# Kernel optimization log

Hardware: AMD Instinct MI355X
Metric: run time of the kernel (lower is better)

## Reference

```python
import jax, jax.numpy as jnp
import numpy as np

Q_OFFSET = 128  # stored quants are in [0,255); subtract to get signed int8 range


def setup_inputs() -> dict:
    key = jax.random.key(0)
    k1, k2, k3, k4 = jax.random.split(key, 4)
    O, NB, BS = 4096, 128, 32  # out_features, num_blocks, block_size (Q8_0)
    x = jax.random.normal(k1, (4, 1024, NB * BS), dtype=jnp.float16)
    q_weight = jax.random.randint(k2, (O, NB, BS), 0, 255, dtype=jnp.int32)
    scales = jax.random.uniform(k3, (O, NB), dtype=jnp.float16) * jnp.float16(0.05)
    bias = jax.random.normal(k4, (O,), dtype=jnp.float16)
    return {"x": x, "q_weight": q_weight, "scales": scales, "bias": bias}


def reference(x, q_weight, scales, bias):
    # GGUF Q8_0-style on-the-fly dequant: w[o, b*32+j] = (q[o,b,j]-128) * scale[o,b]
    q = q_weight.astype(jnp.float16) - jnp.float16(Q_OFFSET)  # [O, NB, BS]
    w = (q * scales[:, :, None]).reshape(scales.shape[0], -1)  # [O, I]
    # linear: y = x @ w^T + bias
    return jnp.einsum('bsi,oi->bso', x, w) + bias
```

## Files before the change

kernel.cpp:

```cpp
#include <hip/hip_runtime.h>
#include <stdint.h>


#define QOFF 128

typedef __bf16 bf16_t;
typedef __bf16 bf16x8 __attribute__((ext_vector_type(8)));
typedef float f32x4 __attribute__((ext_vector_type(4)));

__global__ __launch_bounds__(256) void prep_kernel(
    const int* __restrict__ q, const float* __restrict__ scales,
    const float* __restrict__ X, bf16_t* __restrict__ W,
    bf16_t* __restrict__ Xb, int K, int NB, int nDeq) {
  const int b = blockIdx.x;
  if (b < nDeq) {
    const size_t e = ((size_t)b * 256 + threadIdx.x) * 8;
    const int o = (int)(e / (size_t)K);
    const int i = (int)(e % (size_t)K);
    const float s = scales[o * NB + (i >> 5)];
    int4 a = *(const int4*)(q + e);
    int4 c = *(const int4*)(q + e + 4);
    const int* av = (const int*)&a;
    const int* cv = (const int*)&c;
    bf16x8 t;
#pragma unroll
    for (int j = 0; j < 4; ++j) t[j] = (bf16_t)((float)(av[j] - QOFF) * s);
#pragma unroll
    for (int j = 0; j < 4; ++j) t[4 + j] = (bf16_t)((float)(cv[j] - QOFF) * s);
    *(bf16x8*)(W + e) = t;
  } else {
    const size_t e = ((size_t)(b - nDeq) * 256 + threadIdx.x) * 8;
    float4 a = *(const float4*)(X + e);
    float4 c = *(const float4*)(X + e + 4);
    bf16x8 t;
    t[0] = (bf16_t)a.x; t[1] = (bf16_t)a.y; t[2] = (bf16_t)a.z; t[3] = (bf16_t)a.w;
    t[4] = (bf16_t)c.x; t[5] = (bf16_t)c.y; t[6] = (bf16_t)c.z; t[7] = (bf16_t)c.w;
    *(bf16x8*)(Xb + e) = t;
  }
}

__device__ __forceinline__ void async16(bf16_t* lds, const bf16_t* g) {
  __builtin_amdgcn_global_load_lds(
      (const __attribute__((address_space(1))) unsigned int*)(const void*)g,
      (__attribute__((address_space(3))) unsigned int*)(void*)lds, 16, 0, 0);
}

__global__ __launch_bounds__(256) void gemm_db(
    const bf16_t* __restrict__ A,
    const bf16_t* __restrict__ B,
    const float* __restrict__ bias,
    float* __restrict__ C,
    int M, int N, int K) {
  __shared__ bf16_t lsA[2][128 * 32];
  __shared__ bf16_t lsB[2][128 * 32];

  const int tid = threadIdx.x;
  const int lane = tid & 63;
  const int wave = tid >> 6;
  const int m0 = blockIdx.y * 128;
  const int n0 = blockIdx.x * 128;
  const int wm = (wave >> 1) * 64;
  const int wn = (wave & 1) * 64;
  const int r = lane & 15;
  const int qd = lane >> 4;

  f32x4 acc[4][4] = {};

  const int e0 = tid * 8;
  const int e1 = 2048 + tid * 8;
  const int r0 = e0 >> 5, c0 = e0 & 31;
  const int r1 = e1 >> 5, c1 = e1 & 31;

  const bf16_t* gA0 = A + (size_t)(m0 + r0) * K + c0;
  const bf16_t* gA1 = A + (size_t)(m0 + r1) * K + c1;
  const bf16_t* gB0 = B + (size_t)(n0 + r0) * K + c0;
  const bf16_t* gB1 = B + (size_t)(n0 + r1) * K + c1;

  async16(&lsA[0][e0], gA0);
  async16(&lsA[0][e1], gA1);
  async16(&lsB[0][e0], gB0);
  async16(&lsB[0][e1], gB1);

  int buf = 0;
  for (int k0 = 0; k0 < K; k0 += 32, buf ^= 1) {
    __syncthreads();
    if (k0 + 32 < K) {
      const int nk = k0 + 32;
      async16(&lsA[buf ^ 1][e0], gA0 + nk);
      async16(&lsA[buf ^ 1][e1], gA1 + nk);
      async16(&lsB[buf ^ 1][e0], gB0 + nk);
      async16(&lsB[buf ^ 1][e1], gB1 + nk);
    }

    bf16x8 af[4], bfv[4];
#pragma unroll
    for (int i = 0; i < 4; ++i) {
      af[i] = *(const bf16x8*)&lsA[buf][(wm + i * 16 + r) * 32 + qd * 8];
      bfv[i] = *(const bf16x8*)&lsB[buf][(wn + i * 16 + r) * 32 + qd * 8];
    }
#pragma unroll
    for (int mi = 0; mi < 4; ++mi)
#pragma unroll
      for (int ni = 0; ni < 4; ++ni)
        acc[mi][ni] = __builtin_amdgcn_mfma_f32_16x16x32_bf16(
            af[mi], bfv[ni], acc[mi][ni], 0, 0, 0);
  }

#pragma unroll
  for (int ni = 0; ni < 4; ++ni) {
    const int n = n0 + wn + ni * 16 + r;
    const float bv = bias[n];
#pragma unroll
    for (int mi = 0; mi < 4; ++mi) {
      const int mbase = m0 + wm + mi * 16 + qd * 4;
#pragma unroll
      for (int reg = 0; reg < 4; ++reg) {
        C[(size_t)(mbase + reg) * N + n] = acc[mi][ni][reg] + bv;
      }
    }
  }
}

__global__ __launch_bounds__(256) void gemm_fused(
    const float* __restrict__ Af, const int* __restrict__ q,
    const float* __restrict__ scales, const float* __restrict__ bias,
    float* __restrict__ C, int M, int N, int K, int NB) {
  __shared__ bf16_t lsA[128 * 32];
  __shared__ bf16_t lsB[128 * 32];

  const int tid = threadIdx.x;
  const int lane = tid & 63;
  const int wave = tid >> 6;
  const int m0 = blockIdx.y * 128;
  const int n0 = blockIdx.x * 128;
  const int wm = (wave >> 1) * 64;
  const int wn = (wave & 1) * 64;
  const int r = lane & 15;
  const int qd = lane >> 4;

  const int e = tid * 16;
  const int row = e >> 5;
  const int col = e & 31;

  const float* gAf = Af + (size_t)(m0 + row) * K + col;
  const int* gQ = q + (size_t)(n0 + row) * K + col;
  const float* gS = scales + (size_t)(n0 + row) * NB;

  f32x4 acc[4][4] = {};

  for (int k0 = 0; k0 < K; k0 += 32) {
    bf16x8 a0, a1, b0, b1;
    {
      float4 f0 = *(const float4*)(gAf + k0);
      float4 f1 = *(const float4*)(gAf + k0 + 4);
      float4 f2 = *(const float4*)(gAf + k0 + 8);
      float4 f3 = *(const float4*)(gAf + k0 + 12);
      a0[0] = (bf16_t)f0.x; a0[1] = (bf16_t)f0.y; a0[2] = (bf16_t)f0.z; a0[3] = (bf16_t)f0.w;
      a0[4] = (bf16_t)f1.x; a0[5] = (bf16_t)f1.y; a0[6] = (bf16_t)f1.z; a0[7] = (bf16_t)f1.w;
      a1[0] = (bf16_t)f2.x; a1[1] = (bf16_t)f2.y; a1[2] = (bf16_t)f2.z; a1[3] = (bf16_t)f2.w;
      a1[4] = (bf16_t)f3.x; a1[5] = (bf16_t)f3.y; a1[6] = (bf16_t)f3.z; a1[7] = (bf16_t)f3.w;
    }
    {
      const float s = gS[k0 >> 5];
      int qv[16];
      *(int4*)&qv[0] = *(const int4*)(gQ + k0);
      *(int4*)&qv[4] = *(const int4*)(gQ + k0 + 4);
      *(int4*)&qv[8] = *(const int4*)(gQ + k0 + 8);
      *(int4*)&qv[12] = *(const int4*)(gQ + k0 + 12);
#pragma unroll
      for (int j = 0; j < 8; ++j) b0[j] = (bf16_t)((float)(qv[j] - QOFF) * s);
#pragma unroll
      for (int j = 0; j < 8; ++j)
        b1[j] = (bf16_t)((float)(qv[8 + j] - QOFF) * s);
    }

    __syncthreads();
    *(bf16x8*)&lsA[e] = a0;
    *(bf16x8*)&lsA[e + 8] = a1;
    *(bf16x8*)&lsB[e] = b0;
    *(bf16x8*)&lsB[e + 8] = b1;
    __syncthreads();

    bf16x8 af[4], bfv[4];
#pragma unroll
    for (int i = 0; i < 4; ++i) {
      af[i] = *(const bf16x8*)&lsA[(wm + i * 16 + r) * 32 + qd * 8];
      bfv[i] = *(const bf16x8*)&lsB[(wn + i * 16 + r) * 32 + qd * 8];
    }
#pragma unroll
    for (int mi = 0; mi < 4; ++mi)
#pragma unroll
      for (int ni = 0; ni < 4; ++ni)
        acc[mi][ni] = __builtin_amdgcn_mfma_f32_16x16x32_bf16(
            af[mi], bfv[ni], acc[mi][ni], 0, 0, 0);
  }

#pragma unroll
  for (int ni = 0; ni < 4; ++ni) {
    const int n = n0 + wn + ni * 16 + r;
    const float bv = bias[n];
#pragma unroll
    for (int mi = 0; mi < 4; ++mi) {
      const int mbase = m0 + wm + mi * 16 + qd * 4;
#pragma unroll
      for (int reg = 0; reg < 4; ++reg) {
        C[(size_t)(mbase + reg) * N + n] = acc[mi][ni][reg] + bv;
      }
    }
  }
}

extern "C" void kernel_launch(void* const* d_in, const int* in_sizes, int n_in,
                              void* d_out, int out_size, void* d_ws,
                              size_t ws_size, hipStream_t stream) {
  const float* x = (const float*)d_in[0];
  const int* qw = (const int*)d_in[1];
  const float* scales = (const float*)d_in[2];
  const float* bias = (const float*)d_in[3];
  float* out = (float*)d_out;

  const int O = in_sizes[3];
  const int K = in_sizes[1] / O;
  const int NB = in_sizes[2] / O;
  const int M = in_sizes[0] / K;
  (void)n_in; (void)out_size;

  const size_t Wbytes = (size_t)O * K * sizeof(bf16_t);
  const size_t Xbytes = (size_t)M * K * sizeof(bf16_t);
  dim3 grid(O / 128, M / 128);

  if (ws_size >= Wbytes + Xbytes) {
    bf16_t* W = (bf16_t*)d_ws;
    bf16_t* Xb = (bf16_t*)((char*)d_ws + Wbytes);
    const int nDeq = (int)((size_t)O * K / 2048);
    const int nCvt = (int)((size_t)M * K / 2048);
    prep_kernel<<<nDeq + nCvt, 256, 0, stream>>>(qw, scales, x, W, Xb, K, NB,
                                                 nDeq);
    gemm_db<<<grid, 256, 0, stream>>>(Xb, W, bias, out, M, O, K);
  } else {
    gemm_fused<<<grid, 256, 0, stream>>>(x, qw, scales, bias, out, M, O, K,
                                         NB);
  }
}
```

Measured before the change: 355.8 us.

## Add triple-buffered async-LDS GEMM with partial vmcnt waits

Adds a three-stage LDS pipeline GEMM kernel. It issues global-to-LDS loads two tiles ahead and waits with an explicit s_waitcnt that leaves the newest stage's loads in flight, followed by a raw s_barrier. The aim is to stop stalling on every outstanding load at each iteration, as the double-buffered __syncthreads loop does, and so overlap memory latency with MFMA work. In exchange, LDS use per block rises to 48KB, which may lower occupancy, and correctness depends on the hand-coded waitcnt encoding. The kernel is dispatched only when the K-iteration count fits the 3-way unrolled steady state; otherwise the old kernel runs.

```diff
diff --git a/kernel.cpp b/kernel.cpp
--- a/kernel.cpp
+++ b/kernel.cpp
@@ -7,6 +7,9 @@
 typedef __bf16 bf16_t;
 typedef __bf16 bf16x8 __attribute__((ext_vector_type(8)));
 typedef float f32x4 __attribute__((ext_vector_type(4)));
+
+#define WAIT_VM4_LGKM0 0x0074
+#define WAIT_VM0_LGKM0 0x0070
 
 __global__ __launch_bounds__(256) void prep_kernel(
     const int* __restrict__ q, const float* __restrict__ scales,
@@ -45,14 +48,14 @@
       (__attribute__((address_space(3))) unsigned int*)(void*)lds, 16, 0, 0);
 }
 
-__global__ __launch_bounds__(256) void gemm_db(
+__global__ __launch_bounds__(256) void gemm_pipe(
     const bf16_t* __restrict__ A,
     const bf16_t* __restrict__ B,
     const float* __restrict__ bias,
     float* __restrict__ C,
     int M, int N, int K) {
-  __shared__ bf16_t lsA[2][128 * 32];
-  __shared__ bf16_t lsB[2][128 * 32];
+  __shared__ bf16_t lsA[3][128 * 32];
+  __shared__ bf16_t lsB[3][128 * 32];
 
   const int tid = threadIdx.x;
   const int lane = tid & 63;
@@ -76,6 +79,95 @@
   const bf16_t* gB0 = B + (size_t)(n0 + r0) * K + c0;
   const bf16_t* gB1 = B + (size_t)(n0 + r1) * K + c1;
 
+  auto issue = [&](int s, int koff) {
+    async16(&lsA[s][e0], gA0 + koff);
+    async16(&lsA[s][e1], gA1 + koff);
+    async16(&lsB[s][e0], gB0 + koff);
+    async16(&lsB[s][e1], gB1 + koff);
+  };
+  auto compute = [&](int s) {
+    bf16x8 af[4], bfv[4];
+#pragma unroll
+    for (int i = 0; i < 4; ++i) {
+      af[i] = *(const bf16x8*)&lsA[s][(wm + i * 16 + r) * 32 + qd * 8];
+      bfv[i] = *(const bf16x8*)&lsB[s][(wn + i * 16 + r) * 32 + qd * 8];
+    }
+#pragma unroll
+    for (int mi = 0; mi < 4; ++mi)
+#pragma unroll
+      for (int ni = 0; ni < 4; ++ni)
+        acc[mi][ni] = __builtin_amdgcn_mfma_f32_16x16x32_bf16(
+            af[mi], bfv[ni], acc[mi][ni], 0, 0, 0);
+  };
+
+  const int ITERS = K / 32;
+
+  issue(0, 0);
+  issue(1, 32);
+  __builtin_amdgcn_s_waitcnt(WAIT_VM4_LGKM0);
+  __builtin_amdgcn_s_barrier();
+
+  int k = 0;
+  const int steady = (ITERS - 2) / 3;
+  for (int j = 0; j < steady; ++j) {
+#pragma unroll
+    for (int u = 0; u < 3; ++u) {
+      issue((u + 2) % 3, (k + 2) * 32);
+      compute(u);
+      __builtin_amdgcn_s_waitcnt(WAIT_VM4_LGKM0);
+      __builtin_amdgcn_s_barrier();
+      ++k;
+    }
+  }
+  compute(0);
+  __builtin_amdgcn_s_waitcnt(WAIT_VM0_LGKM0);
+  __builtin_amdgcn_s_barrier();
+  compute(1);
+
+#pragma unroll
+  for (int ni = 0; ni < 4; ++ni) {
+    const int n = n0 + wn + ni * 16 + r;
+    const float bv = bias[n];
+#pragma unroll
+    for (int mi = 0; mi < 4; ++mi) {
+      const int mbase = m0 + wm + mi * 16 + qd * 4;
+#pragma unroll
+      for (int reg = 0; reg < 4; ++reg) {
+        C[(size_t)(mbase + reg) * N + n] = acc[mi][ni][reg] + bv;
+      }
+    }
+  }
+}
+
+__global__ __launch_bounds__(256) void gemm_db(
+    const bf16_t* __restrict__ A, const bf16_t* __restrict__ B,
+    const float* __restrict__ bias, float* __restrict__ C, int M, int N,
+    int K) {
+  __shared__ bf16_t lsA[2][128 * 32];
+  __shared__ bf16_t lsB[2][128 * 32];
+
+  const int tid = threadIdx.x;
+  const int lane = tid & 63;
+  const int wave = tid >> 6;
+  const int m0 = blockIdx.y * 128;
+  const int n0 = blockIdx.x * 128;
+  const int wm = (wave >> 1) * 64;
+  const int wn = (wave & 1) * 64;
+  const int r = lane & 15;
+  const int qd = lane >> 4;
+
+  f32x4 acc[4][4] = {};
+
+  const int e0 = tid * 8;
+  const int e1 = 2048 + tid * 8;
+  const int r0 = e0 >> 5, c0 = e0 & 31;
+  const int r1 = e1 >> 5, c1 = e1 & 31;
+
+  const bf16_t* gA0 = A + (size_t)(m0 + r0) * K + c0;
+  const bf16_t* gA1 = A + (size_t)(m0 + r1) * K + c1;
+  const bf16_t* gB0 = B + (size_t)(n0 + r0) * K + c0;
+  const bf16_t* gB1 = B + (size_t)(n0 + r1) * K + c1;
+
   async16(&lsA[0][e0], gA0);
   async16(&lsA[0][e1], gA1);
   async16(&lsB[0][e0], gB0);
@@ -91,7 +183,6 @@
       async16(&lsB[buf ^ 1][e0], gB0 + nk);
       async16(&lsB[buf ^ 1][e1], gB1 + nk);
     }
-
     bf16x8 af[4], bfv[4];
 #pragma unroll
     for (int i = 0; i < 4; ++i) {
@@ -236,7 +327,12 @@
     const int nCvt = (int)((size_t)M * K / 2048);
     prep_kernel<<<nDeq + nCvt, 256, 0, stream>>>(qw, scales, x, W, Xb, K, NB,
                                                  nDeq);
-    gemm_db<<<grid, 256, 0, stream>>>(Xb, W, bias, out, M, O, K);
+    const int iters = K / 32;
+    if (iters >= 5 && (iters - 2) % 3 == 0) {
+      gemm_pipe<<<grid, 256, 0, stream>>>(Xb, W, bias, out, M, O, K);
+    } else {
+      gemm_db<<<grid, 256, 0, stream>>>(Xb, W, bias, out, M, O, K);
+    }
   } else {
     gemm_fused<<<grid, 256, 0, stream>>>(x, qw, scales, bias, out, M, O, K,
                                          NB);
```

After: 349.1 us. About the same (-1.9%).
